# Optimization experiments

Hardware: AMD Instinct MI355X
Metric: run time of the kernel (lower is better)

The kernel has to match this reference:

```python
import jax, jax.numpy as jnp
import numpy as np

N = 100000
E = 1600000
IN_DIM, HIDDEN, OUT_DIM, HEADS = 256, 128, 64, 2
NEG_SLOPE = 0.2


def setup_inputs() -> dict:
    key = jax.random.key(0)
    ks = jax.random.split(key, 10)
    inv = lambda d: 1.0 / np.sqrt(d)
    return {
        "x": jax.random.normal(ks[0], (N, IN_DIM), dtype=jnp.float32),
        "edge_index": jax.random.randint(ks[1], (2, E), 0, N, dtype=jnp.int64),
        "W1": jax.random.normal(ks[2], (IN_DIM, HEADS * HIDDEN), dtype=jnp.float32) * inv(IN_DIM),
        "att_src1": jax.random.normal(ks[3], (HEADS, HIDDEN), dtype=jnp.float32) * inv(HIDDEN),
        "att_dst1": jax.random.normal(ks[4], (HEADS, HIDDEN), dtype=jnp.float32) * inv(HIDDEN),
        "b1": jnp.zeros((HIDDEN,), dtype=jnp.float32),
        "W2": jax.random.normal(ks[5], (HIDDEN, OUT_DIM), dtype=jnp.float32) * inv(HIDDEN),
        "att_src2": jax.random.normal(ks[6], (1, OUT_DIM), dtype=jnp.float32) * inv(OUT_DIM),
        "att_dst2": jax.random.normal(ks[7], (1, OUT_DIM), dtype=jnp.float32) * inv(OUT_DIM),
        "b2": jnp.zeros((OUT_DIM,), dtype=jnp.float32),
    }


def gat_conv(x, W, att_src, att_dst, bias, src, dst, heads, ch):
    # Linear transform: [N, H, C]
    h = (x @ W).reshape(N, heads, ch)
    # Per-node attention logits: [N, H]
    a_s = jnp.einsum("nhc,hc->nh", h, att_src)
    a_d = jnp.einsum("nhc,hc->nh", h, att_dst)
    # Edge-wise scores (self-loops already in src/dst): [E', H]
    e = jax.nn.leaky_relu(a_s[src] + a_d[dst], NEG_SLOPE)
    # Segment softmax over incoming edges of each dst node
    m = jax.ops.segment_max(e, dst, num_segments=N)
    alpha = jnp.exp(e - m[dst])
    denom = jax.ops.segment_sum(alpha, dst, num_segments=N)
    alpha = alpha / denom[dst]
    # Weighted scatter-add aggregation: [N, H, C]
    out = jax.ops.segment_sum(alpha[:, :, None] * h[src], dst, num_segments=N)
    # concat=False -> mean over heads, then bias
    return out.mean(axis=1) + bias


def reference(x, edge_index, W1, att_src1, att_dst1, b1, W2, att_src2, att_dst2, b2):
    # PyG GATConv default: add self-loops
    loop = jnp.arange(N, dtype=edge_index.dtype)
    src = jnp.concatenate([edge_index[0], loop])
    dst = jnp.concatenate([edge_index[1], loop])
    h = gat_conv(x, W1, att_src1, att_dst1, b1, src, dst, HEADS, HIDDEN)
    h = jax.nn.relu(h)  # dropout is identity in eval mode
    out = gat_conv(h, W2, att_src2, att_dst2, b2, src, dst, 1, OUT_DIM)
    return out
```

## Files before the change

### kernel.cpp

```cpp
#include <hip/hip_runtime.h>
#include <hip/hip_bf16.h>
#include <cstdint>
#include <cstddef>

#define IN_D 256
#define HID 128
#define OUT_D 64
#define NSLOPE 0.2f
#define PAD 128

typedef __attribute__((ext_vector_type(8))) short bf16x8;
typedef __attribute__((ext_vector_type(4))) float f32x4;
typedef __attribute__((ext_vector_type(8))) unsigned short u16x8;
typedef unsigned short u16;

static inline int cdiv(long long a, long long b) { return (int)((a + b - 1) / b); }

__device__ __forceinline__ float lrelu(float v) { return v >= 0.f ? v : NSLOPE * v; }

__device__ __forceinline__ u16 f2bf(float f) {
  unsigned u = __float_as_uint(f);
  return (u16)((u + 0x7FFFu + ((u >> 16) & 1u)) >> 16);
}
__device__ __forceinline__ float bf2f(u16 h) {
  return __uint_as_float((unsigned)h << 16);
}

__global__ void k_prep(const float* __restrict__ W1, u16* __restrict__ WThi,
                       u16* __restrict__ WTlo, const float* __restrict__ W2,
                       u16* __restrict__ W2Thi, u16* __restrict__ W2Tlo) {
  int idx = blockIdx.x * 256 + threadIdx.x;
  if (idx < IN_D * IN_D) {
    int k = idx >> 8, n = idx & 255;
    float f = W1[idx];
    u16 h = f2bf(f);
    WThi[n * IN_D + k] = h;
    WTlo[n * IN_D + k] = f2bf(f - bf2f(h));
  }
  int idx2 = idx - IN_D * IN_D;
  if (idx2 >= 0 && idx2 < HID * OUT_D) {
    int k = idx2 >> 6, n = idx2 & 63;
    float f = W2[idx2];
    u16 h = f2bf(f);
    W2Thi[n * HID + k] = h;
    W2Tlo[n * HID + k] = f2bf(f - bf2f(h));
  }
}

__launch_bounds__(512)
__global__ void k_gemm1buck(const float* __restrict__ x, const u16* __restrict__ WThi,
                            const u16* __restrict__ WTlo,
                            const float* __restrict__ as1, const float* __restrict__ ad1,
                            u16* __restrict__ hb, float* __restrict__ a_s,
                            float* __restrict__ a_d, int N,
                            const int* __restrict__ ei, int E,
                            int* __restrict__ cnt, int* __restrict__ colp,
                            int G1, int G2) {
  __shared__ u16 ldsb[2][10240];
  int bid = blockIdx.x;
  int m2 = (G1 < G2 ? G1 : G2) * 2;
  int type, tb;
  if (bid < m2) { type = bid & 1; tb = bid >> 1; }
  else { int ex = bid - m2; type = (G1 > G2) ? 0 : 1; tb = m2 / 2 + ex; }

  if (type == 1) {
    int base = tb * 2048 + threadIdx.x;
    int sv[4], dv[4]; bool vv[4];
    #pragma unroll
    for (int q = 0; q < 4; ++q) {
      int i = base + q * 512;
      vv[q] = i < E;
      int ic = vv[q] ? i : 0;
      sv[q] = ei[ic];
      dv[q] = ei[E + ic];
    }
    int pv[4];
    #pragma unroll
    for (int q = 0; q < 4; ++q)
      pv[q] = vv[q] ? atomicAdd(&cnt[dv[q]], 1) : PAD;
    #pragma unroll
    for (int q = 0; q < 4; ++q)
      if (pv[q] < PAD) colp[(size_t)dv[q] * PAD + pv[q]] = sv[q];
    return;
  }

  int tid = threadIdx.x;
  int w = tid >> 6, l = tid & 63;
  int l15 = l & 15, l4 = l >> 4;
  int rowbase = tb * 128 + w * 16;
  int row = rowbase + l15;
  int rowc = (row < N) ? row : (N - 1);
  const float* xp = x + (size_t)rowc * IN_D + l4 * 8;

  f32x4 acc[16];
  #pragma unroll
  for (int t = 0; t < 16; ++t) acc[t] = (f32x4){0.f, 0.f, 0.f, 0.f};

  const int ridx = (l15 * 5 + l4) * 8;

  for (int kk = 0; kk < 8; ++kk) {
    __syncthreads();
    #pragma unroll
    for (int it = 0; it < 2; ++it) {
      int c = tid + it * 512;
      int n = c >> 2, ch = c & 3;
      size_t soff = (size_t)n * IN_D + kk * 32 + ch * 8;
      uint4 vh = *(const uint4*)(WThi + soff);
      uint4 vl = *(const uint4*)(WTlo + soff);
      int dsl = (n * 5 + ch) * 8;
      *(uint4*)&ldsb[0][dsl] = vh;
      *(uint4*)&ldsb[1][dsl] = vl;
    }
    __syncthreads();

    f32x4 v0 = *(const f32x4*)(xp + kk * 32);
    f32x4 v1 = *(const f32x4*)(xp + kk * 32 + 4);
    bf16x8 ah, al;
    #pragma unroll
    for (int j = 0; j < 4; ++j) {
      u16 h0 = f2bf(v0[j]);
      ah[j] = (short)h0; al[j] = (short)f2bf(v0[j] - bf2f(h0));
      u16 h1 = f2bf(v1[j]);
      ah[j + 4] = (short)h1; al[j + 4] = (short)f2bf(v1[j] - bf2f(h1));
    }
    #pragma unroll
    for (int t = 0; t < 16; ++t) {
      bf16x8 bh = *(const bf16x8*)&ldsb[0][ridx + t * 640];
      bf16x8 bl = *(const bf16x8*)&ldsb[1][ridx + t * 640];
      acc[t] = __builtin_amdgcn_mfma_f32_16x16x32_bf16(ah, bh, acc[t], 0, 0, 0);
      acc[t] = __builtin_amdgcn_mfma_f32_16x16x32_bf16(al, bh, acc[t], 0, 0, 0);
      acc[t] = __builtin_amdgcn_mfma_f32_16x16x32_bf16(ah, bl, acc[t], 0, 0, 0);
    }
  }

  #pragma unroll
  for (int r = 0; r < 4; ++r) {
    int rr = rowbase + l4 * 4 + r;
    if (rr < N) {
      u16* hp = hb + (size_t)rr * IN_D + l15;
      #pragma unroll
      for (int t = 0; t < 16; ++t) hp[t * 16] = f2bf(acc[t][r]);
    }
  }
  float asv[16], adv[16];
  #pragma unroll
  for (int t = 0; t < 16; ++t) { asv[t] = as1[t * 16 + l15]; adv[t] = ad1[t * 16 + l15]; }
  float ps0[4] = {}, ps1[4] = {}, pd0[4] = {}, pd1[4] = {};
  #pragma unroll
  for (int t = 0; t < 16; ++t) {
    #pragma unroll
    for (int r = 0; r < 4; ++r) {
      float v = acc[t][r];
      if (t < 8) { ps0[r] += v * asv[t]; pd0[r] += v * adv[t]; }
      else       { ps1[r] += v * asv[t]; pd1[r] += v * adv[t]; }
    }
  }
  #pragma unroll
  for (int r = 0; r < 4; ++r) {
    #pragma unroll
    for (int o = 1; o < 16; o <<= 1) {
      ps0[r] += __shfl_xor(ps0[r], o); ps1[r] += __shfl_xor(ps1[r], o);
      pd0[r] += __shfl_xor(pd0[r], o); pd1[r] += __shfl_xor(pd1[r], o);
    }
    int rr = rowbase + l4 * 4 + r;
    if (l15 == 0 && rr < N) {
      a_s[rr * 2] = ps0[r]; a_s[rr * 2 + 1] = ps1[r];
      a_d[rr * 2] = pd0[r]; a_d[rr * 2 + 1] = pd1[r];
    }
  }
}

__launch_bounds__(256)
__global__ void k_fagg1g2(const int* __restrict__ cnt, const int* __restrict__ colp,
                          const float* __restrict__ a_s, const float* __restrict__ a_d,
                          const u16* __restrict__ hb, const float* __restrict__ b1,
                          const u16* __restrict__ W2Thi, const u16* __restrict__ W2Tlo,
                          const float* __restrict__ as2, const float* __restrict__ ad2,
                          u16* __restrict__ h2b, float* __restrict__ a_s2,
                          float* __restrict__ a_d2, int N) {
  __shared__ float rowLds[16][132];
  __shared__ float red[2][16][4];
  int tid = threadIdx.x;
  int wid = tid >> 6, lane = tid & 63;
  int base = blockIdx.x * 16;

  int half = lane >> 5;
  int l5 = lane & 31;
  int head = l5 >> 4;

  for (int rr = 0; rr < 4; ++rr) {
    int ln = wid * 4 + rr;
    int n = base + ln;
    if (n >= N) { if (lane < 16) for (int q = 0; q < 8; ++q) rowLds[ln][lane * 8 + q] = 0.f; continue; }
    size_t begb = (size_t)n * PAD;
    int cn = cnt[n]; cn = (cn < PAD) ? cn : PAD;
    float ad0 = a_d[2 * n], ad1 = a_d[2 * n + 1];
    float myAd = head ? ad1 : ad0;

    float sacc = 0.f;
    float accv[8] = {};
    if (half == 0) {
      float2 asn = *(const float2*)&a_s[2 * (size_t)n];
      float wv = __expf(lrelu((head ? asn.y : asn.x) + myAd));
      sacc = wv;
      const u16x8 hv = *(const u16x8*)&hb[(size_t)n * IN_D + l5 * 8];
      #pragma unroll
      for (int q = 0; q < 8; ++q) accv[q] = wv * bf2f(hv[q]);
    }
    #pragma unroll 4
    for (int j = 0; j < cn; j += 2) {
      int jj = j + half;
      bool valid = jj < cn;
      int jc = valid ? jj : 0;
      int sidx = colp[begb + jc];
      float2 asv = *(const float2*)&a_s[2 * (size_t)sidx];
      float e = (head ? asv.y : asv.x) + myAd;
      float wv = __expf(lrelu(e));
      wv = valid ? wv : 0.f;
      sacc += wv;
      const u16x8 hv = *(const u16x8*)&hb[(size_t)sidx * IN_D + l5 * 8];
      #pragma unroll
      for (int q = 0; q < 8; ++q) accv[q] += wv * bf2f(hv[q]);
    }
    sacc += __shfl_xor(sacc, 32);
    float myScale = 0.5f / sacc;
    #pragma unroll
    for (int q = 0; q < 8; ++q) {
      accv[q] *= myScale;
      accv[q] += __shfl_xor(accv[q], 16);
      accv[q] += __shfl_xor(accv[q], 32);
    }
    if (lane < 16) {
      #pragma unroll
      for (int q = 0; q < 8; ++q) rowLds[ln][lane * 8 + q] = accv[q];
    }
  }
  __syncthreads();

  int l15 = lane & 15, l4 = lane >> 4;
  f32x4 acc2 = (f32x4){0.f, 0.f, 0.f, 0.f};
  #pragma unroll
  for (int kk = 0; kk < 4; ++kk) {
    int k0 = kk * 32 + l4 * 8;
    f32x4 bv0 = *(const f32x4*)(b1 + k0);
    f32x4 bv1 = *(const f32x4*)(b1 + k0 + 4);
    bf16x8 ah, al;
    #pragma unroll
    for (int j = 0; j < 4; ++j) {
      float u0 = rowLds[l15][k0 + j] + bv0[j]; u0 = (u0 > 0.f) ? u0 : 0.f;
      u16 h0 = f2bf(u0);
      ah[j] = (short)h0; al[j] = (short)f2bf(u0 - bf2f(h0));
      float u1 = rowLds[l15][k0 + 4 + j] + bv1[j]; u1 = (u1 > 0.f) ? u1 : 0.f;
      u16 h1 = f2bf(u1);
      ah[j + 4] = (short)h1; al[j + 4] = (short)f2bf(u1 - bf2f(h1));
    }
    size_t boff = (size_t)(wid * 16 + l15) * HID + k0;
    bf16x8 bh = *(const bf16x8*)(W2Thi + boff);
    bf16x8 bl = *(const bf16x8*)(W2Tlo + boff);
    acc2 = __builtin_amdgcn_mfma_f32_16x16x32_bf16(ah, bh, acc2, 0, 0, 0);
    acc2 = __builtin_amdgcn_mfma_f32_16x16x32_bf16(al, bh, acc2, 0, 0, 0);
    acc2 = __builtin_amdgcn_mfma_f32_16x16x32_bf16(ah, bl, acc2, 0, 0, 0);
  }

  float asv = as2[wid * 16 + l15], adv = ad2[wid * 16 + l15];
  float ps[4], pd[4];
  #pragma unroll
  for (int r = 0; r < 4; ++r) {
    int n = base + l4 * 4 + r;
    if (n < N) h2b[(size_t)n * OUT_D + wid * 16 + l15] = f2bf(acc2[r]);
    ps[r] = acc2[r] * asv; pd[r] = acc2[r] * adv;
    #pragma unroll
    for (int o = 1; o < 16; o <<= 1) { ps[r] += __shfl_xor(ps[r], o); pd[r] += __shfl_xor(pd[r], o); }
    if (l15 == 0) { red[0][l4 * 4 + r][wid] = ps[r]; red[1][l4 * 4 + r][wid] = pd[r]; }
  }
  __syncthreads();
  if (tid < 32) {
    int ln = tid >> 1, kind = tid & 1;
    int n = base + ln;
    if (n < N) {
      float v = red[kind][ln][0] + red[kind][ln][1] + red[kind][ln][2] + red[kind][ln][3];
      if (kind == 0) a_s2[n] = v; else a_d2[n] = v;
    }
  }
}

__launch_bounds__(256)
__global__ void k_fagg2(const int* __restrict__ cnt, const int* __restrict__ colp,
                        const float* __restrict__ a_s, const float* __restrict__ a_d,
                        const u16* __restrict__ h2b, const float* __restrict__ b2,
                        float* __restrict__ out, int N) {
  int gid = blockIdx.x * blockDim.x + threadIdx.x;
  int n = gid >> 6, lane = gid & 63;
  if (n >= N) return;
  size_t beg = (size_t)n * PAD;
  int cn = cnt[n]; cn = (cn < PAD) ? cn : PAD;
  float ad = a_d[n];

  int g = lane >> 3, l3 = lane & 7;
  float sacc = 0.f;
  float accv[8] = {};
  if (g == 0) {
    float w = __expf(lrelu(a_s[n] + ad));
    sacc = w;
    const u16x8 hv = *(const u16x8*)&h2b[(size_t)n * OUT_D + l3 * 8];
    #pragma unroll
    for (int q = 0; q < 8; ++q) accv[q] = w * bf2f(hv[q]);
  }
  #pragma unroll 4
  for (int j = 0; j < cn; j += 8) {
    int jj = j + g;
    bool valid = jj < cn;
    int jc = valid ? jj : 0;
    int sidx = colp[beg + jc];
    float w = __expf(lrelu(a_s[sidx] + ad));
    w = valid ? w : 0.f;
    sacc += w;
    const u16x8 hv = *(const u16x8*)&h2b[(size_t)sidx * OUT_D + l3 * 8];
    #pragma unroll
    for (int q = 0; q < 8; ++q) accv[q] += w * bf2f(hv[q]);
  }
  sacc += __shfl_xor(sacc, 8);
  sacc += __shfl_xor(sacc, 16);
  sacc += __shfl_xor(sacc, 32);
  float rcp = 1.f / sacc;
  #pragma unroll
  for (int q = 0; q < 8; ++q) {
    accv[q] *= rcp;
    accv[q] += __shfl_xor(accv[q], 8);
    accv[q] += __shfl_xor(accv[q], 16);
    accv[q] += __shfl_xor(accv[q], 32);
  }
  if (lane < 8) {
    float* op = out + (size_t)n * OUT_D + lane * 8;
    const float* bp = b2 + lane * 8;
    float4 o0 = {accv[0] + bp[0], accv[1] + bp[1], accv[2] + bp[2], accv[3] + bp[3]};
    float4 o1 = {accv[4] + bp[4], accv[5] + bp[5], accv[6] + bp[6], accv[7] + bp[7]};
    *(float4*)op = o0;
    *(float4*)(op + 4) = o1;
  }
}

extern "C" void kernel_launch(void* const* d_in, const int* in_sizes, int n_in,
                              void* d_out, int out_size, void* d_ws, size_t ws_size,
                              hipStream_t stream) {
  const float* x    = (const float*)d_in[0];
  const int*   ei   = (const int*)d_in[1];
  const float* W1   = (const float*)d_in[2];
  const float* as1w = (const float*)d_in[3];
  const float* ad1w = (const float*)d_in[4];
  const float* b1   = (const float*)d_in[5];
  const float* W2   = (const float*)d_in[6];
  const float* as2w = (const float*)d_in[7];
  const float* ad2w = (const float*)d_in[8];
  const float* b2   = (const float*)d_in[9];
  float* out = (float*)d_out;

  const int N  = in_sizes[0] / IN_D;
  const int E  = in_sizes[1] / 2;

  float* ws = (float*)d_ws;
  size_t off = 0;
  u16*   hb1  = (u16*)(ws + off); off += (size_t)N * IN_D / 2;
  u16*   h2b  = (u16*)(ws + off); off += (size_t)N * OUT_D / 2;
  float* a_s1 = ws + off; off += (size_t)N * 2;
  float* a_d1 = ws + off; off += (size_t)N * 2;
  float* a_s2 = ws + off; off += N;
  float* a_d2 = ws + off; off += N;
  int*   cnt  = (int*)(ws + off); off += N;
  int*   colp = (int*)(ws + off); off += (size_t)N * PAD;
  u16*   WThi = (u16*)(ws + off); off += (IN_D * IN_D) / 2;
  u16*   WTlo = (u16*)(ws + off); off += (IN_D * IN_D) / 2;
  u16*   W2Thi = (u16*)(ws + off); off += (HID * OUT_D) / 2;
  u16*   W2Tlo = (u16*)(ws + off); off += (HID * OUT_D) / 2;

  hipMemsetAsync(cnt, 0, (size_t)N * sizeof(int), stream);

  k_prep<<<cdiv(IN_D * IN_D + HID * OUT_D, 256), 256, 0, stream>>>(
      W1, WThi, WTlo, W2, W2Thi, W2Tlo);

  const int G1 = cdiv(N, 128);
  const int G2 = cdiv(E, 2048);
  k_gemm1buck<<<G1 + G2, 512, 0, stream>>>(x, WThi, WTlo, as1w, ad1w, hb1, a_s1, a_d1, N,
                                           ei, E, cnt, colp, G1, G2);

  k_fagg1g2<<<cdiv(N, 16), 256, 0, stream>>>(cnt, colp, a_s1, a_d1, hb1, b1,
                                             W2Thi, W2Tlo, as2w, ad2w, h2b, a_s2, a_d2, N);

  k_fagg2<<<cdiv((long long)N * 64, 256), 256, 0, stream>>>(cnt, colp, a_s2, a_d2, h2b, b2, out, N);
}
```

Measured before the change: 329.6 us.

## Split destination edge buckets per XCD with workgroup-scope atomics

The CSR-like bucket build now keeps a separate counter and 32-slot edge list per destination node for each XCD, chosen by reading the hardware XCC_ID. The atomics drop to workgroup scope so that bucket fills avoid device-wide coherent atomics across XCDs. Both aggregation kernels walk the 8 sub-buckets: layer 1 has each half-wave take 4 segments, and layer 2 has each 8-lane group take one segment. The trade-offs are a larger counter memset, edge lists spread over more cache lines, uneven per-segment loop lengths causing divergence, and reliance on same-XCD workgroups seeing each other's workgroup-scope atomics through the shared L2.

```diff
diff --git a/kernel.cpp b/kernel.cpp
--- a/kernel.cpp
+++ b/kernel.cpp
@@ -7,7 +7,8 @@
 #define HID 128
 #define OUT_D 64
 #define NSLOPE 0.2f
-#define PAD 128
+#define NXCD 8
+#define PAD2 32
 
 typedef __attribute__((ext_vector_type(8))) short bf16x8;
 typedef __attribute__((ext_vector_type(4))) float f32x4;
@@ -54,7 +55,7 @@
                             u16* __restrict__ hb, float* __restrict__ a_s,
                             float* __restrict__ a_d, int N,
                             const int* __restrict__ ei, int E,
-                            int* __restrict__ cnt, int* __restrict__ colp,
+                            int* __restrict__ cnt8, int* __restrict__ colp,
                             int G1, int G2) {
   __shared__ u16 ldsb[2][10240];
   int bid = blockIdx.x;
@@ -64,6 +65,9 @@
   else { int ex = bid - m2; type = (G1 > G2) ? 0 : 1; tb = m2 / 2 + ex; }
 
   if (type == 1) {
+    unsigned xcc;
+    asm volatile("s_getreg_b32 %0, hwreg(HW_REG_XCC_ID)" : "=s"(xcc));
+    xcc &= (NXCD - 1);
     int base = tb * 2048 + threadIdx.x;
     int sv[4], dv[4]; bool vv[4];
     #pragma unroll
@@ -77,10 +81,12 @@
     int pv[4];
     #pragma unroll
     for (int q = 0; q < 4; ++q)
-      pv[q] = vv[q] ? atomicAdd(&cnt[dv[q]], 1) : PAD;
+      pv[q] = vv[q] ? __hip_atomic_fetch_add(&cnt8[(size_t)dv[q] * NXCD + xcc], 1,
+                                             __ATOMIC_RELAXED, __HIP_MEMORY_SCOPE_WORKGROUP)
+                    : PAD2;
     #pragma unroll
     for (int q = 0; q < 4; ++q)
-      if (pv[q] < PAD) colp[(size_t)dv[q] * PAD + pv[q]] = sv[q];
+      if (pv[q] < PAD2) colp[((size_t)dv[q] * NXCD + xcc) * PAD2 + pv[q]] = sv[q];
     return;
   }
 
@@ -171,7 +177,7 @@
 }
 
 __launch_bounds__(256)
-__global__ void k_fagg1g2(const int* __restrict__ cnt, const int* __restrict__ colp,
+__global__ void k_fagg1g2(const int* __restrict__ cnt8, const int* __restrict__ colp,
                           const float* __restrict__ a_s, const float* __restrict__ a_d,
                           const u16* __restrict__ hb, const float* __restrict__ b1,
                           const u16* __restrict__ W2Thi, const u16* __restrict__ W2Tlo,
@@ -192,8 +198,6 @@
     int ln = wid * 4 + rr;
     int n = base + ln;
     if (n >= N) { if (lane < 16) for (int q = 0; q < 8; ++q) rowLds[ln][lane * 8 + q] = 0.f; continue; }
-    size_t begb = (size_t)n * PAD;
-    int cn = cnt[n]; cn = (cn < PAD) ? cn : PAD;
     float ad0 = a_d[2 * n], ad1 = a_d[2 * n + 1];
     float myAd = head ? ad1 : ad0;
 
@@ -207,20 +211,21 @@
       #pragma unroll
       for (int q = 0; q < 8; ++q) accv[q] = wv * bf2f(hv[q]);
     }
-    #pragma unroll 4
-    for (int j = 0; j < cn; j += 2) {
-      int jj = j + half;
-      bool valid = jj < cn;
-      int jc = valid ? jj : 0;
-      int sidx = colp[begb + jc];
-      float2 asv = *(const float2*)&a_s[2 * (size_t)sidx];
-      float e = (head ? asv.y : asv.x) + myAd;
-      float wv = __expf(lrelu(e));
-      wv = valid ? wv : 0.f;
-      sacc += wv;
-      const u16x8 hv = *(const u16x8*)&hb[(size_t)sidx * IN_D + l5 * 8];
-      #pragma unroll
-      for (int q = 0; q < 8; ++q) accv[q] += wv * bf2f(hv[q]);
+    #pragma unroll
+    for (int xs = 0; xs < 4; ++xs) {
+      int xseg = xs * 2 + half;
+      int cn = cnt8[(size_t)n * NXCD + xseg]; cn = (cn < PAD2) ? cn : PAD2;
+      const int* cp = colp + ((size_t)n * NXCD + xseg) * PAD2;
+      for (int j = 0; j < cn; ++j) {
+        int sidx = cp[j];
+        float2 asv = *(const float2*)&a_s[2 * (size_t)sidx];
+        float e = (head ? asv.y : asv.x) + myAd;
+        float wv = __expf(lrelu(e));
+        sacc += wv;
+        const u16x8 hv = *(const u16x8*)&hb[(size_t)sidx * IN_D + l5 * 8];
+        #pragma unroll
+        for (int q = 0; q < 8; ++q) accv[q] += wv * bf2f(hv[q]);
+      }
     }
     sacc += __shfl_xor(sacc, 32);
     float myScale = 0.5f / sacc;
@@ -285,18 +290,19 @@
 }
 
 __launch_bounds__(256)
-__global__ void k_fagg2(const int* __restrict__ cnt, const int* __restrict__ colp,
+__global__ void k_fagg2(const int* __restrict__ cnt8, const int* __restrict__ colp,
                         const float* __restrict__ a_s, const float* __restrict__ a_d,
                         const u16* __restrict__ h2b, const float* __restrict__ b2,
                         float* __restrict__ out, int N) {
   int gid = blockIdx.x * blockDim.x + threadIdx.x;
   int n = gid >> 6, lane = gid & 63;
   if (n >= N) return;
-  size_t beg = (size_t)n * PAD;
-  int cn = cnt[n]; cn = (cn < PAD) ? cn : PAD;
   float ad = a_d[n];
 
   int g = lane >> 3, l3 = lane & 7;
+  int cn = cnt8[(size_t)n * NXCD + g]; cn = (cn < PAD2) ? cn : PAD2;
+  const int* cp = colp + ((size_t)n * NXCD + g) * PAD2;
+
   float sacc = 0.f;
   float accv[8] = {};
   if (g == 0) {
@@ -306,14 +312,9 @@
     #pragma unroll
     for (int q = 0; q < 8; ++q) accv[q] = w * bf2f(hv[q]);
   }
-  #pragma unroll 4
-  for (int j = 0; j < cn; j += 8) {
-    int jj = j + g;
-    bool valid = jj < cn;
-    int jc = valid ? jj : 0;
-    int sidx = colp[beg + jc];
+  for (int j = 0; j < cn; ++j) {
+    int sidx = cp[j];
     float w = __expf(lrelu(a_s[sidx] + ad));
-    w = valid ? w : 0.f;
     sacc += w;
     const u16x8 hv = *(const u16x8*)&h2b[(size_t)sidx * OUT_D + l3 * 8];
     #pragma unroll
@@ -366,14 +367,14 @@
   float* a_d1 = ws + off; off += (size_t)N * 2;
   float* a_s2 = ws + off; off += N;
   float* a_d2 = ws + off; off += N;
-  int*   cnt  = (int*)(ws + off); off += N;
-  int*   colp = (int*)(ws + off); off += (size_t)N * PAD;
+  int*   cnt8 = (int*)(ws + off); off += (size_t)N * NXCD;
+  int*   colp = (int*)(ws + off); off += (size_t)N * NXCD * PAD2;
   u16*   WThi = (u16*)(ws + off); off += (IN_D * IN_D) / 2;
   u16*   WTlo = (u16*)(ws + off); off += (IN_D * IN_D) / 2;
   u16*   W2Thi = (u16*)(ws + off); off += (HID * OUT_D) / 2;
   u16*   W2Tlo = (u16*)(ws + off); off += (HID * OUT_D) / 2;
 
-  hipMemsetAsync(cnt, 0, (size_t)N * sizeof(int), stream);
+  hipMemsetAsync(cnt8, 0, (size_t)N * NXCD * sizeof(int), stream);
 
   k_prep<<<cdiv(IN_D * IN_D + HID * OUT_D, 256), 256, 0, stream>>>(
       W1, WThi, WTlo, W2, W2Thi, W2Tlo);
@@ -381,10 +382,10 @@
   const int G1 = cdiv(N, 128);
   const int G2 = cdiv(E, 2048);
   k_gemm1buck<<<G1 + G2, 512, 0, stream>>>(x, WThi, WTlo, as1w, ad1w, hb1, a_s1, a_d1, N,
-                                           ei, E, cnt, colp, G1, G2);
-
-  k_fagg1g2<<<cdiv(N, 16), 256, 0, stream>>>(cnt, colp, a_s1, a_d1, hb1, b1,
+                                           ei, E, cnt8, colp, G1, G2);
+
+  k_fagg1g2<<<cdiv(N, 16), 256, 0, stream>>>(cnt8, colp, a_s1, a_d1, hb1, b1,
                                              W2Thi, W2Tlo, as2w, ad2w, h2b, a_s2, a_d2, N);
 
-  k_fagg2<<<cdiv((long long)N * 64, 256), 256, 0, stream>>>(cnt, colp, a_s2, a_d2, h2b, b2, out, N);
-}
+  k_fagg2<<<cdiv((long long)N * 64, 256), 256, 0, stream>>>(cnt8, colp, a_s2, a_d2, h2b, b2, out, N);
+}
```

After: 477.5 us. 1.45x slower.

## Build compact CSR via two-pass bucketed counting sort instead of padded buckets

Applied to the files above, without the earlier changes.

Replaces the per-destination padded bucket (128 slots per node, filled with global atomics inside the GEMM launch) with a two-pass counting sort. The first pass buckets edges into 1024-node superblocks using shared-memory histograms. The second pass sorts each superblock locally in LDS and writes a compact row-offset/column CSR. This is meant to cut global atomic contention and the large, sparse padded colp footprint, and it gives the aggregation kernels contiguous neighbor lists. In exchange it adds two kernel launches, an intermediate int2 buffer, and a serial prefix over superblock counts in each block. It also stops overlapping edge bucketing with the GEMM, and superblocks holding more than SBCAP edges are silently truncated.

```diff
diff --git a/kernel.cpp b/kernel.cpp
--- a/kernel.cpp
+++ b/kernel.cpp
@@ -7,7 +7,7 @@
 #define HID 128
 #define OUT_D 64
 #define NSLOPE 0.2f
-#define PAD 128
+#define SBCAP 20480
 
 typedef __attribute__((ext_vector_type(8))) short bf16x8;
 typedef __attribute__((ext_vector_type(4))) float f32x4;
@@ -17,6 +17,7 @@
 static inline int cdiv(long long a, long long b) { return (int)((a + b - 1) / b); }
 
 __device__ __forceinline__ float lrelu(float v) { return v >= 0.f ? v : NSLOPE * v; }
+__device__ __forceinline__ int imin(int a, int b) { return a < b ? a : b; }
 
 __device__ __forceinline__ u16 f2bf(float f) {
   unsigned u = __float_as_uint(f);
@@ -47,47 +48,105 @@
   }
 }
 
+__launch_bounds__(256)
+__global__ void k_sort1(const int* __restrict__ ei, int E,
+                        int* __restrict__ sbCount, int2* __restrict__ st1) {
+  __shared__ int hist[128], gb[128], cur[128];
+  int tid = threadIdx.x;
+  if (tid < 128) hist[tid] = 0;
+  __syncthreads();
+  int base = blockIdx.x * 2048 + tid;
+  int sv[8], dv[8]; bool vv[8];
+  #pragma unroll
+  for (int q = 0; q < 8; ++q) {
+    int i = base + q * 256;
+    vv[q] = i < E;
+    int ic = vv[q] ? i : 0;
+    sv[q] = ei[ic];
+    dv[q] = ei[E + ic];
+  }
+  #pragma unroll
+  for (int q = 0; q < 8; ++q)
+    if (vv[q]) atomicAdd(&hist[dv[q] >> 10], 1);
+  __syncthreads();
+  if (tid < 128) {
+    int h = hist[tid];
+    gb[tid] = h ? atomicAdd(&sbCount[tid], h) : 0;
+    cur[tid] = 0;
+  }
+  __syncthreads();
+  #pragma unroll
+  for (int q = 0; q < 8; ++q)
+    if (vv[q]) {
+      int sb = dv[q] >> 10;
+      int r = atomicAdd(&cur[sb], 1);
+      int slot = gb[sb] + r;
+      if (slot < SBCAP) st1[(size_t)sb * SBCAP + slot] = make_int2(sv[q], dv[q]);
+    }
+}
+
+__launch_bounds__(256)
+__global__ void k_sort2(const int* __restrict__ sbCount, const int2* __restrict__ st1,
+                        int* __restrict__ ro, int* __restrict__ col, int N) {
+  __shared__ int hist2[1024], pref[1024], cur[1024];
+  __shared__ int sc[256];
+  __shared__ int gbaseS, cntS;
+  int tid = threadIdx.x;
+  int sb = blockIdx.x;
+  int nb0 = sb << 10;
+  if (tid == 0) {
+    int g = 0;
+    for (int b = 0; b < sb; ++b) g += imin(sbCount[b], SBCAP);
+    gbaseS = g;
+    cntS = imin(sbCount[sb], SBCAP);
+  }
+  for (int t = tid; t < 1024; t += 256) hist2[t] = 0;
+  __syncthreads();
+  int gbase = gbaseS, cnt = cntS;
+  const int2* sp = st1 + (size_t)sb * SBCAP;
+  for (int j = tid; j < cnt; j += 256) atomicAdd(&hist2[sp[j].y - nb0], 1);
+  __syncthreads();
+  int a0 = hist2[tid * 4], a1 = hist2[tid * 4 + 1],
+      a2 = hist2[tid * 4 + 2], a3 = hist2[tid * 4 + 3];
+  int s4 = a0 + a1 + a2 + a3;
+  sc[tid] = s4; __syncthreads();
+  for (int o = 1; o < 256; o <<= 1) {
+    int add = (tid >= o) ? sc[tid - o] : 0;
+    __syncthreads();
+    sc[tid] += add;
+    __syncthreads();
+  }
+  int eb = sc[tid] - s4;
+  pref[tid * 4] = eb;
+  pref[tid * 4 + 1] = eb + a0;
+  pref[tid * 4 + 2] = eb + a0 + a1;
+  pref[tid * 4 + 3] = eb + a0 + a1 + a2;
+  __syncthreads();
+  for (int t = tid; t < 1024; t += 256) {
+    cur[t] = pref[t];
+    int n = nb0 + t;
+    if (n < N) ro[n] = gbase + pref[t];
+  }
+  if (sb == (int)gridDim.x - 1 && tid == 0) ro[N] = gbase + cnt;
+  __syncthreads();
+  for (int j = tid; j < cnt; j += 256) {
+    int2 e = sp[j];
+    int r = atomicAdd(&cur[e.y - nb0], 1);
+    col[gbase + r] = e.x;
+  }
+}
+
 __launch_bounds__(512)
-__global__ void k_gemm1buck(const float* __restrict__ x, const u16* __restrict__ WThi,
-                            const u16* __restrict__ WTlo,
-                            const float* __restrict__ as1, const float* __restrict__ ad1,
-                            u16* __restrict__ hb, float* __restrict__ a_s,
-                            float* __restrict__ a_d, int N,
-                            const int* __restrict__ ei, int E,
-                            int* __restrict__ cnt, int* __restrict__ colp,
-                            int G1, int G2) {
+__global__ void k_gemm1(const float* __restrict__ x, const u16* __restrict__ WThi,
+                        const u16* __restrict__ WTlo,
+                        const float* __restrict__ as1, const float* __restrict__ ad1,
+                        u16* __restrict__ hb, float* __restrict__ a_s,
+                        float* __restrict__ a_d, int N) {
   __shared__ u16 ldsb[2][10240];
-  int bid = blockIdx.x;
-  int m2 = (G1 < G2 ? G1 : G2) * 2;
-  int type, tb;
-  if (bid < m2) { type = bid & 1; tb = bid >> 1; }
-  else { int ex = bid - m2; type = (G1 > G2) ? 0 : 1; tb = m2 / 2 + ex; }
-
-  if (type == 1) {
-    int base = tb * 2048 + threadIdx.x;
-    int sv[4], dv[4]; bool vv[4];
-    #pragma unroll
-    for (int q = 0; q < 4; ++q) {
-      int i = base + q * 512;
-      vv[q] = i < E;
-      int ic = vv[q] ? i : 0;
-      sv[q] = ei[ic];
-      dv[q] = ei[E + ic];
-    }
-    int pv[4];
-    #pragma unroll
-    for (int q = 0; q < 4; ++q)
-      pv[q] = vv[q] ? atomicAdd(&cnt[dv[q]], 1) : PAD;
-    #pragma unroll
-    for (int q = 0; q < 4; ++q)
-      if (pv[q] < PAD) colp[(size_t)dv[q] * PAD + pv[q]] = sv[q];
-    return;
-  }
-
   int tid = threadIdx.x;
   int w = tid >> 6, l = tid & 63;
   int l15 = l & 15, l4 = l >> 4;
-  int rowbase = tb * 128 + w * 16;
+  int rowbase = blockIdx.x * 128 + w * 16;
   int row = rowbase + l15;
   int rowc = (row < N) ? row : (N - 1);
   const float* xp = x + (size_t)rowc * IN_D + l4 * 8;
@@ -171,7 +230,7 @@
 }
 
 __launch_bounds__(256)
-__global__ void k_fagg1g2(const int* __restrict__ cnt, const int* __restrict__ colp,
+__global__ void k_fagg1g2(const int* __restrict__ ro, const int* __restrict__ col,
                           const float* __restrict__ a_s, const float* __restrict__ a_d,
                           const u16* __restrict__ hb, const float* __restrict__ b1,
                           const u16* __restrict__ W2Thi, const u16* __restrict__ W2Tlo,
@@ -192,8 +251,7 @@
     int ln = wid * 4 + rr;
     int n = base + ln;
     if (n >= N) { if (lane < 16) for (int q = 0; q < 8; ++q) rowLds[ln][lane * 8 + q] = 0.f; continue; }
-    size_t begb = (size_t)n * PAD;
-    int cn = cnt[n]; cn = (cn < PAD) ? cn : PAD;
+    int beg = ro[n], end = ro[n + 1];
     float ad0 = a_d[2 * n], ad1 = a_d[2 * n + 1];
     float myAd = head ? ad1 : ad0;
 
@@ -208,11 +266,10 @@
       for (int q = 0; q < 8; ++q) accv[q] = wv * bf2f(hv[q]);
     }
     #pragma unroll 4
-    for (int j = 0; j < cn; j += 2) {
+    for (int j = beg; j < end; j += 2) {
       int jj = j + half;
-      bool valid = jj < cn;
-      int jc = valid ? jj : 0;
-      int sidx = colp[begb + jc];
+      bool valid = jj < end;
+      int sidx = col[valid ? jj : beg];
       float2 asv = *(const float2*)&a_s[2 * (size_t)sidx];
       float e = (head ? asv.y : asv.x) + myAd;
       float wv = __expf(lrelu(e));
@@ -285,15 +342,14 @@
 }
 
 __launch_bounds__(256)
-__global__ void k_fagg2(const int* __restrict__ cnt, const int* __restrict__ colp,
+__global__ void k_fagg2(const int* __restrict__ ro, const int* __restrict__ col,
                         const float* __restrict__ a_s, const float* __restrict__ a_d,
                         const u16* __restrict__ h2b, const float* __restrict__ b2,
                         float* __restrict__ out, int N) {
   int gid = blockIdx.x * blockDim.x + threadIdx.x;
   int n = gid >> 6, lane = gid & 63;
   if (n >= N) return;
-  size_t beg = (size_t)n * PAD;
-  int cn = cnt[n]; cn = (cn < PAD) ? cn : PAD;
+  int beg = ro[n], end = ro[n + 1];
   float ad = a_d[n];
 
   int g = lane >> 3, l3 = lane & 7;
@@ -307,11 +363,10 @@
     for (int q = 0; q < 8; ++q) accv[q] = w * bf2f(hv[q]);
   }
   #pragma unroll 4
-  for (int j = 0; j < cn; j += 8) {
+  for (int j = beg; j < end; j += 8) {
     int jj = j + g;
-    bool valid = jj < cn;
-    int jc = valid ? jj : 0;
-    int sidx = colp[beg + jc];
+    bool valid = jj < end;
+    int sidx = col[valid ? jj : beg];
     float w = __expf(lrelu(a_s[sidx] + ad));
     w = valid ? w : 0.f;
     sacc += w;
@@ -355,8 +410,9 @@
   const float* b2   = (const float*)d_in[9];
   float* out = (float*)d_out;
 
-  const int N  = in_sizes[0] / IN_D;
-  const int E  = in_sizes[1] / 2;
+  const int N   = in_sizes[0] / IN_D;
+  const int E   = in_sizes[1] / 2;
+  const int NSB = cdiv(N, 1024);
 
   float* ws = (float*)d_ws;
   size_t off = 0;
@@ -366,25 +422,27 @@
   float* a_d1 = ws + off; off += (size_t)N * 2;
   float* a_s2 = ws + off; off += N;
   float* a_d2 = ws + off; off += N;
-  int*   cnt  = (int*)(ws + off); off += N;
-  int*   colp = (int*)(ws + off); off += (size_t)N * PAD;
+  int*   sbCount = (int*)(ws + off); off += 128;
+  int2*  st1  = (int2*)(ws + off); off += (size_t)NSB * SBCAP * 2;
+  int*   ro   = (int*)(ws + off); off += (size_t)N + 1;
+  int*   col  = (int*)(ws + off); off += E;
   u16*   WThi = (u16*)(ws + off); off += (IN_D * IN_D) / 2;
   u16*   WTlo = (u16*)(ws + off); off += (IN_D * IN_D) / 2;
   u16*   W2Thi = (u16*)(ws + off); off += (HID * OUT_D) / 2;
   u16*   W2Tlo = (u16*)(ws + off); off += (HID * OUT_D) / 2;
 
-  hipMemsetAsync(cnt, 0, (size_t)N * sizeof(int), stream);
+  hipMemsetAsync(sbCount, 0, 128 * sizeof(int), stream);
 
   k_prep<<<cdiv(IN_D * IN_D + HID * OUT_D, 256), 256, 0, stream>>>(
       W1, WThi, WTlo, W2, W2Thi, W2Tlo);
 
-  const int G1 = cdiv(N, 128);
-  const int G2 = cdiv(E, 2048);
-  k_gemm1buck<<<G1 + G2, 512, 0, stream>>>(x, WThi, WTlo, as1w, ad1w, hb1, a_s1, a_d1, N,
-                                           ei, E, cnt, colp, G1, G2);
-
-  k_fagg1g2<<<cdiv(N, 16), 256, 0, stream>>>(cnt, colp, a_s1, a_d1, hb1, b1,
+  k_sort1<<<cdiv(E, 2048), 256, 0, stream>>>(ei, E, sbCount, st1);
+  k_sort2<<<NSB, 256, 0, stream>>>(sbCount, st1, ro, col, N);
+
+  k_gemm1<<<cdiv(N, 128), 512, 0, stream>>>(x, WThi, WTlo, as1w, ad1w, hb1, a_s1, a_d1, N);
+
+  k_fagg1g2<<<cdiv(N, 16), 256, 0, stream>>>(ro, col, a_s1, a_d1, hb1, b1,
                                              W2Thi, W2Tlo, as2w, ad2w, h2b, a_s2, a_d2, N);
 
-  k_fagg2<<<cdiv((long long)N * 64, 256), 256, 0, stream>>>(cnt, colp, a_s2, a_d2, h2b, b2, out, N);
-}
+  k_fagg2<<<cdiv((long long)N * 64, 256), 256, 0, stream>>>(ro, col, a_s2, a_d2, h2b, b2, out, N);
+}
```

Result: slower. 339.1 us (+2.9%).
